# Performance work log

Measured on AMD Instinct MI355X. Metric: run time of the kernel, lower is better.

The kernel has to match this reference:

```python
import jax, jax.numpy as jnp
import numpy as np

HEADS = 6
DIM_HEAD = 64
SCALE = DIM_HEAD ** -0.5
BN_EPS = 1e-5


def _dw_pw(x, w_dw, gamma, beta, mean, var, w_pw, stride):
    """Depthwise 3x3 conv (groups=C) -> BatchNorm (inference) -> 1x1 pointwise conv."""
    C = x.shape[1]
    y = jax.lax.conv_general_dilated(
        x, w_dw, window_strides=(stride, stride), padding=((1, 1), (1, 1)),
        dimension_numbers=('NCHW', 'OIHW', 'NCHW'), feature_group_count=C)
    inv = gamma / jnp.sqrt(var + BN_EPS)
    y = y * inv[None, :, None, None] + (beta - mean * inv)[None, :, None, None]
    # 1x1 conv as einsum: w_pw is [O, C]
    return jnp.einsum('bchw,oc->bohw', y, w_pw)


def setup_inputs() -> dict:
    key = jax.random.key(0)
    ks = jax.random.split(key, 10)
    B, C, H, W = 32, 384, 32, 32
    inner = HEADS * DIM_HEAD  # 384
    ws = 0.05  # weight scale to keep attention logits sane
    return {
        'x': jax.random.normal(ks[0], (B, C, H, W), jnp.float32),
        'q_dw': jax.random.normal(ks[1], (C, 1, 3, 3), jnp.float32) * ws,
        'q_gamma': jnp.ones((C,), jnp.float32),
        'q_beta': jnp.zeros((C,), jnp.float32),
        'q_mean': jax.random.normal(ks[2], (C,), jnp.float32) * 0.1,
        'q_var': jax.random.uniform(ks[3], (C,), jnp.float32) + 0.5,
        'q_pw': jax.random.normal(ks[4], (inner, C), jnp.float32) * ws,
        'kv_dw': jax.random.normal(ks[5], (C, 1, 3, 3), jnp.float32) * ws,
        'kv_gamma': jnp.ones((C,), jnp.float32),
        'kv_beta': jnp.zeros((C,), jnp.float32),
        'kv_mean': jax.random.normal(ks[6], (C,), jnp.float32) * 0.1,
        'kv_var': jax.random.uniform(ks[7], (C,), jnp.float32) + 0.5,
        'kv_pw': jax.random.normal(ks[8], (2 * inner, C), jnp.float32) * ws,
        'out_w': jax.random.normal(ks[9], (C, inner), jnp.float32) * ws,
        'out_b': jnp.zeros((C,), jnp.float32),
    }


def reference(x, q_dw, q_gamma, q_beta, q_mean, q_var, q_pw,
              kv_dw, kv_gamma, kv_beta, kv_mean, kv_var, kv_pw,
              out_w, out_b):
    B, C, H, W = x.shape
    h, d = HEADS, DIM_HEAD
    # Q at full resolution, K/V spatially downsampled (stride 2)
    q = _dw_pw(x, q_dw, q_gamma, q_beta, q_mean, q_var, q_pw, stride=1)   # [B, h*d, H, W]
    kv = _dw_pw(x, kv_dw, kv_gamma, kv_beta, kv_mean, kv_var, kv_pw, stride=2)  # [B, 2*h*d, Hk, Wk]
    k, v = jnp.split(kv, 2, axis=1)
    Hk, Wk = k.shape[2], k.shape[3]
    # 'b (h d) x y -> b h (x y) d'
    q = q.reshape(B, h, d, H * W).transpose(0, 1, 3, 2)
    k = k.reshape(B, h, d, Hk * Wk).transpose(0, 1, 3, 2)
    v = v.reshape(B, h, d, Hk * Wk).transpose(0, 1, 3, 2)
    dots = jnp.einsum('bhid,bhjd->bhij', q, k) * SCALE  # [B, h, HW, HkWk]
    attn = jax.nn.softmax(dots, axis=-1)
    out = jnp.einsum('bhij,bhjd->bhid', attn, v)        # [B, h, HW, d]
    # 'b h (x y) d -> b (h d) x y'
    out = out.transpose(0, 1, 3, 2).reshape(B, h * d, H, W)
    # final 1x1 conv projection (dropout is identity, p=0)
    return jnp.einsum('bchw,oc->bohw', out, out_w) + out_b[None, :, None, None]
```

## Files before the change

kernel.cpp:

```cpp
#include <hip/hip_runtime.h>
#include <hip/hip_bf16.h>

#define CIN 384
#define PQ 1024
#define PKV 256
#define HEADS 6
#define DH 64
#define INNER 384
#define ATTN_SCALE 0.125f

typedef __hip_bfloat16 bf16;
typedef unsigned short ushort;
typedef __bf16 bf16x8 __attribute__((ext_vector_type(8)));
typedef float floatx4 __attribute__((ext_vector_type(4)));

__device__ __forceinline__ float b2f(bf16 v) { return __bfloat162float(v); }
__device__ __forceinline__ bf16 f2b(float v) { return __float2bfloat16(v); }
__device__ __forceinline__ ushort f2bu(float v) { bf16 h = __float2bfloat16(v); return *(ushort*)&h; }
__device__ __forceinline__ float ldf(const void* p, size_t i, int isbf) {
    return isbf ? __bfloat162float(((const bf16*)p)[i]) : ((const float*)p)[i];
}
__device__ __forceinline__ void dma16(const bf16* g, bf16* l) {
    __builtin_amdgcn_global_load_lds(
        (const __attribute__((address_space(1))) unsigned int*)g,
        (__attribute__((address_space(3))) unsigned int*)l, 16, 0, 0);
}
__device__ __forceinline__ int probe_isbf(const void* x) {
    const unsigned* u = (const unsigned*)x;
    int cnt = 0;
    for (int i = 0; i < 64; i++) {
        unsigned e = (u[i] >> 7) & 0xFFu;
        cnt += (e >= 100u && e <= 140u) ? 1 : 0;
    }
    return cnt >= 48 ? 1 : 0;
}
__device__ __forceinline__ unsigned cvtpk(float lo, float hi) {
    unsigned r;
    asm("v_cvt_pk_bf16_f32 %0, %1, %2" : "=v"(r) : "v"(lo), "v"(hi));
    return r;
}
__device__ __forceinline__ void halfswap(unsigned a, unsigned b, unsigned& lo, unsigned& hi) {
#if __has_builtin(__builtin_amdgcn_permlane32_swap)
    auto r = __builtin_amdgcn_permlane32_swap(a, b, false, false);
    lo = r[0]; hi = r[1];
#else
    unsigned ax = (unsigned)__shfl_xor((int)a, 32, 64);
    unsigned bx = (unsigned)__shfl_xor((int)b, 32, 64);
    bool lower = (threadIdx.x & 32) == 0;
    lo = lower ? a : bx;
    hi = lower ? ax : b;
#endif
}

template <int STRIDE, int G, int HO, int WO>
__device__ __forceinline__ void dw_bn_body(
        const void* __restrict__ x, const void* __restrict__ wdw,
        const void* __restrict__ gamma, const void* __restrict__ beta,
        const void* __restrict__ mean, const void* __restrict__ var,
        bf16* __restrict__ yt, int isbf, int rg, int c0, int b, int tid,
        char* smem) {
    constexpr int IN_ROWS = (G - 1) * STRIDE + 3;
    constexpr int PT = G * WO;
    float* xs = (float*)smem;
    ushort (*outt)[40] = (ushort (*)[40])smem;

    int ri0 = rg * G * STRIDE - 1;

    const int NCHUNK = 32 * IN_ROWS * 4;
    for (int ch = tid; ch < NCHUNK; ch += 256) {
        int wc = ch & 3;
        int cc = (ch >> 2) & 31;
        int i  = ch >> 7;
        int row = ri0 + i;
        float f[8];
        if (row >= 0 && row < 32) {
            size_t goff = ((size_t)(b * CIN + c0 + cc) * 32 + row) * 32 + wc * 8;
            if (isbf) {
                uint4 v = *(const uint4*)((const bf16*)x + goff);
                const ushort* u = (const ushort*)&v;
#pragma unroll
                for (int j = 0; j < 8; j++) f[j] = __uint_as_float((unsigned)u[j] << 16);
            } else {
                float4 v0 = *(const float4*)((const float*)x + goff);
                float4 v1 = *(const float4*)((const float*)x + goff + 4);
                f[0] = v0.x; f[1] = v0.y; f[2] = v0.z; f[3] = v0.w;
                f[4] = v1.x; f[5] = v1.y; f[6] = v1.z; f[7] = v1.w;
            }
        } else {
#pragma unroll
            for (int j = 0; j < 8; j++) f[j] = 0.f;
        }
        float* rb = xs + ((size_t)(i * 32 + cc)) * 32;
        int key = cc & 7;
        float4 fa = {f[0], f[1], f[2], f[3]};
        float4 fb = {f[4], f[5], f[6], f[7]};
        *(float4*)(rb + ((2 * wc) ^ key) * 4)     = fa;
        *(float4*)(rb + ((2 * wc + 1) ^ key) * 4) = fb;
    }

    int cc = tid & 31;
    int g  = tid >> 5;
    int c  = c0 + cc;
    int key = cc & 7;
    float w9[9];
#pragma unroll
    for (int k = 0; k < 9; k++) w9[k] = ldf(wdw, c * 9 + k, isbf);
    float inv  = ldf(gamma, c, isbf) * rsqrtf(ldf(var, c, isbf) + 1e-5f);
    float bias = ldf(beta, c, isbf) - ldf(mean, c, isbf) * inv;
    __syncthreads();

    float o[STRIDE == 1 ? 32 : 8];
    if (STRIDE == 1) {
#pragma unroll
        for (int p = 0; p < 2; p++) {
            float rf[3][18];
#pragma unroll
            for (int ky = 0; ky < 3; ky++) {
                const float* rb = xs + ((size_t)((g + ky) * 32 + cc)) * 32;
#pragma unroll
                for (int cch = 0; cch < 4; cch++) {
                    float4 v = *(const float4*)(rb + ((4 * p + cch) ^ key) * 4);
                    rf[ky][1 + 4 * cch] = v.x; rf[ky][2 + 4 * cch] = v.y;
                    rf[ky][3 + 4 * cch] = v.z; rf[ky][4 + 4 * cch] = v.w;
                }
                rf[ky][0]  = p ? rb[((3 ^ key) * 4) + 3] : 0.f;
                rf[ky][17] = p ? 0.f : rb[((4 ^ key) * 4) + 0];
            }
#pragma unroll
            for (int j = 0; j < 16; j++) {
                float acc = w9[0] * rf[0][j] + w9[1] * rf[0][j + 1] + w9[2] * rf[0][j + 2]
                          + w9[3] * rf[1][j] + w9[4] * rf[1][j + 1] + w9[5] * rf[1][j + 2]
                          + w9[6] * rf[2][j] + w9[7] * rf[2][j + 1] + w9[8] * rf[2][j + 2];
                o[p * 16 + j] = acc * inv + bias;
            }
        }
    } else {
        int rgrp = g & 3, hf = g >> 2;
        float rf[3][17];
#pragma unroll
        for (int ky = 0; ky < 3; ky++) {
            const float* rb = xs + ((size_t)((2 * rgrp + ky) * 32 + cc)) * 32;
#pragma unroll
            for (int cch = 0; cch < 4; cch++) {
                float4 v = *(const float4*)(rb + ((4 * hf + cch) ^ key) * 4);
                rf[ky][1 + 4 * cch] = v.x; rf[ky][2 + 4 * cch] = v.y;
                rf[ky][3 + 4 * cch] = v.z; rf[ky][4 + 4 * cch] = v.w;
            }
            rf[ky][0] = hf ? rb[((3 ^ key) * 4) + 3] : 0.f;
        }
#pragma unroll
        for (int j = 0; j < 8; j++) {
            float acc = w9[0] * rf[0][2 * j] + w9[1] * rf[0][2 * j + 1] + w9[2] * rf[0][2 * j + 2]
                      + w9[3] * rf[1][2 * j] + w9[4] * rf[1][2 * j + 1] + w9[5] * rf[1][2 * j + 2]
                      + w9[6] * rf[2][2 * j] + w9[7] * rf[2][2 * j + 1] + w9[8] * rf[2][2 * j + 2];
            o[j] = acc * inv + bias;
        }
    }
    __syncthreads();

    if (STRIDE == 1) {
#pragma unroll
        for (int wo = 0; wo < 32; wo++) outt[g * WO + wo][cc] = f2bu(o[wo]);
    } else {
        int rgrp = g & 3, hf = g >> 2;
#pragma unroll
        for (int j = 0; j < 8; j++) outt[rgrp * 16 + hf * 8 + j][cc] = f2bu(o[j]);
    }
    __syncthreads();

    const size_t pbase = (size_t)b * (HO * WO) + (size_t)rg * G * WO;
    for (int chk = tid; chk < PT * 4; chk += 256) {
        int k = chk & 3, p = chk >> 2;
        uint4 v = *(const uint4*)&outt[p][k * 8];
        *(uint4*)(yt + (pbase + p) * CIN + c0 + k * 8) = v;
    }
}

__global__ __launch_bounds__(256) void dw_bn_all(
        const void* __restrict__ x,
        const void* __restrict__ q_dw, const void* __restrict__ q_gamma,
        const void* __restrict__ q_beta, const void* __restrict__ q_mean,
        const void* __restrict__ q_var, bf16* __restrict__ yqt,
        const void* __restrict__ kv_dw, const void* __restrict__ kv_gamma,
        const void* __restrict__ kv_beta, const void* __restrict__ kv_mean,
        const void* __restrict__ kv_var, bf16* __restrict__ ykvt,
        const void* __restrict__ w0, const void* __restrict__ w1,
        const void* __restrict__ w2, bf16* __restrict__ wdst) {
    __shared__ __align__(16) char smem[40960];
    int isbf = probe_isbf(x);
    int rg = blockIdx.x;
    int y  = blockIdx.y;
    int b  = blockIdx.z;
    int tid = threadIdx.x;

    if (y < 12) {
        dw_bn_body<1, 8, 32, 32>(x, q_dw, q_gamma, q_beta, q_mean, q_var,
                                 yqt, isbf, rg, y * 32, b, tid, smem);
    } else if (y == 12) {
        const int n0 = INNER * CIN, n1 = 2 * INNER * CIN, n2 = INNER * CIN;
        const int total = n0 + n1 + n2;
        for (int i = (b * 4 + rg) * 256 + tid; i < total; i += 32768) {
            float v;
            if (i < n0) v = ldf(w0, i, isbf);
            else if (i < n0 + n1) v = ldf(w1, i - n0, isbf);
            else v = ldf(w2, i - n0 - n1, isbf);
            wdst[i] = f2b(v);
        }
    } else {
        dw_bn_body<2, 4, 16, 16>(x, kv_dw, kv_gamma, kv_beta, kv_mean, kv_var,
                                 ykvt, isbf, rg, (y - 13) * 32, b, tid, smem);
    }
}

__global__ __launch_bounds__(256, 3) void mfma_pw_qkv(
        const bf16* __restrict__ qpw, const bf16* __restrict__ yqt,
        bf16* __restrict__ qalt,
        const bf16* __restrict__ kvpw, const bf16* __restrict__ ykvt,
        bf16* __restrict__ kalt, bf16* __restrict__ valt) {
    __shared__ __align__(16) bf16 As[2][4096];
    __shared__ __align__(16) bf16 Bs[2][4096];
    int tid = threadIdx.x;
    int wave = tid >> 6, lane = tid & 63;
    int l15 = lane & 15, quad = lane >> 4;
    int wm = wave & 1, wn = wave >> 1;

    int bid = blockIdx.x;
    int P, b, p0, o0;
    const bf16 *asrc0, *bsrc0;
    bf16* outq;
    if (bid < 768) {
        int m = bid;
        int p0t = m & 7; m >>= 3;
        int o0t = m % 3; b = m / 3;
        P = 1024; p0 = p0t * 128; o0 = o0t * 128;
        asrc0 = yqt; bsrc0 = qpw; outq = qalt;
    } else {
        int m = bid - 768;
        int p0t = m & 1; m >>= 1;
        int o0t = m % 6; b = m / 6;
        P = 256; p0 = p0t * 128; o0 = o0t * 128;
        asrc0 = ykvt; bsrc0 = kvpw; outq = kalt;
    }

    const bf16* asrc = asrc0 + ((size_t)b * P + p0) * CIN;
    const bf16* bsrc = bsrc0 + (size_t)o0 * CIN;

    int srow = (lane >> 2);
    int sc   = lane & 3;
    auto stage = [&](int step, int buf) {
#pragma unroll
        for (int it = 0; it < 2; it++) {
            int row = wave * 32 + it * 16 + srow;
            int g = sc ^ (row & 3);
            size_t goff = (size_t)row * CIN + step * 32 + g * 8;
            dma16(asrc + goff, &As[buf][(wave * 2 + it) * 512]);
            dma16(bsrc + goff, &Bs[buf][(wave * 2 + it) * 512]);
        }
    };

    floatx4 acc[4][4];
#pragma unroll
    for (int pt = 0; pt < 4; pt++)
#pragma unroll
        for (int ot = 0; ot < 4; ot++) acc[pt][ot] = (floatx4){0.f, 0.f, 0.f, 0.f};

    stage(0, 0);
    __syncthreads();
    for (int s = 0; s < CIN / 32; s++) {
        int buf = s & 1;
        if (s < CIN / 32 - 1) stage(s + 1, buf ^ 1);
        bf16x8 af[4], bw[4];
        int slot = (quad ^ (l15 & 3)) * 8;
#pragma unroll
        for (int pt = 0; pt < 4; pt++)
            af[pt] = *(const bf16x8*)&As[buf][(wm * 64 + pt * 16 + l15) * 32 + slot];
#pragma unroll
        for (int ot = 0; ot < 4; ot++)
            bw[ot] = *(const bf16x8*)&Bs[buf][(wn * 64 + ot * 16 + l15) * 32 + slot];
#pragma unroll
        for (int pt = 0; pt < 4; pt++)
#pragma unroll
            for (int ot = 0; ot < 4; ot++)
                acc[pt][ot] = __builtin_amdgcn_mfma_f32_16x16x32_bf16(af[pt], bw[ot], acc[pt][ot], 0, 0, 0);
        __syncthreads();
    }

    int pw0 = p0 + wm * 64, ow0 = o0 + wn * 64;
#pragma unroll
    for (int ot = 0; ot < 4; ot++) {
        int o = ow0 + ot * 16 + l15;
        if (o < INNER) {
            int h = o >> 6, d = o & 63;
            bf16* base = outq + ((size_t)(b * HEADS + h) * P) * 64 + d;
#pragma unroll
            for (int pt = 0; pt < 4; pt++)
#pragma unroll
                for (int r = 0; r < 4; r++)
                    base[(size_t)(pw0 + pt * 16 + quad * 4 + r) * 64] = f2b(acc[pt][ot][r]);
        } else {
            int ch = o - INNER;
            bf16* base = valt + ((size_t)b * INNER + ch) * PKV;
#pragma unroll
            for (int pt = 0; pt < 4; pt++)
#pragma unroll
                for (int r = 0; r < 4; r++)
                    base[pw0 + pt * 16 + quad * 4 + r] = f2b(acc[pt][ot][r]);
        }
    }
}

__global__ __launch_bounds__(256, 3) void mfma_pw_out(
        const bf16* __restrict__ wt, const bf16* __restrict__ yt,
        const void* __restrict__ bias, void* __restrict__ out0,
        const void* __restrict__ xprobe) {
    __shared__ __align__(16) bf16 As[2][4096];
    __shared__ __align__(16) bf16 Bs[2][4096];
    const int P = PQ, O = CIN;
    int tid = threadIdx.x;
    int wave = tid >> 6, lane = tid & 63;
    int l15 = lane & 15, quad = lane >> 4;
    int wm = wave & 1, wn = wave >> 1;
    int b = blockIdx.z;
    int p0 = blockIdx.x * 128;
    int o0 = blockIdx.y * 128;

    const bf16* asrc = yt + ((size_t)b * P + p0) * CIN;
    const bf16* bsrc = wt + (size_t)o0 * CIN;

    int srow = (lane >> 2);
    int sc   = lane & 3;
    auto stage = [&](int step, int buf) {
#pragma unroll
        for (int it = 0; it < 2; it++) {
            int row = wave * 32 + it * 16 + srow;
            int g = sc ^ (row & 3);
            size_t goff = (size_t)row * CIN + step * 32 + g * 8;
            dma16(asrc + goff, &As[buf][(wave * 2 + it) * 512]);
            dma16(bsrc + goff, &Bs[buf][(wave * 2 + it) * 512]);
        }
    };

    floatx4 acc[4][4];
#pragma unroll
    for (int pt = 0; pt < 4; pt++)
#pragma unroll
        for (int ot = 0; ot < 4; ot++) acc[pt][ot] = (floatx4){0.f, 0.f, 0.f, 0.f};

    stage(0, 0);
    __syncthreads();
    for (int s = 0; s < CIN / 32; s++) {
        int buf = s & 1;
        if (s < CIN / 32 - 1) stage(s + 1, buf ^ 1);
        bf16x8 af[4], bw[4];
        int slot = (quad ^ (l15 & 3)) * 8;
#pragma unroll
        for (int pt = 0; pt < 4; pt++)
            af[pt] = *(const bf16x8*)&As[buf][(wm * 64 + pt * 16 + l15) * 32 + slot];
#pragma unroll
        for (int ot = 0; ot < 4; ot++)
            bw[ot] = *(const bf16x8*)&Bs[buf][(wn * 64 + ot * 16 + l15) * 32 + slot];
#pragma unroll
        for (int pt = 0; pt < 4; pt++)
#pragma unroll
            for (int ot = 0; ot < 4; ot++)
                acc[pt][ot] = __builtin_amdgcn_mfma_f32_16x16x32_bf16(af[pt], bw[ot], acc[pt][ot], 0, 0, 0);
        __syncthreads();
    }

    int pw0 = p0 + wm * 64, ow0 = o0 + wn * 64;
    int isbf = probe_isbf(xprobe);
#pragma unroll
    for (int ot = 0; ot < 4; ot++) {
        int o = ow0 + ot * 16 + l15;
        float bv = ldf(bias, o, isbf);
#pragma unroll
        for (int pt = 0; pt < 4; pt++) {
            int p = pw0 + pt * 16 + quad * 4;
            size_t idx = ((size_t)b * O + o) * P + p;
            if (!isbf) {
                float4 v4 = {acc[pt][ot][0] + bv, acc[pt][ot][1] + bv,
                             acc[pt][ot][2] + bv, acc[pt][ot][3] + bv};
                *(float4*)((float*)out0 + idx) = v4;
            } else {
                ushort4 u4 = {f2bu(acc[pt][ot][0] + bv), f2bu(acc[pt][ot][1] + bv),
                              f2bu(acc[pt][ot][2] + bv), f2bu(acc[pt][ot][3] + bv)};
                *(ushort4*)((bf16*)out0 + idx) = u4;
            }
        }
    }
}

#define QKT(S, Q0, Q1)                                                              \
    do {                                                                            \
        floatx4 z_ = (floatx4){0.f, 0.f, 0.f, 0.f};                                 \
        _Pragma("unroll")                                                           \
        for (int jt_ = 0; jt_ < 16; jt_++) {                                        \
            int j_ = jt_ * 16 + l15;                                                \
            bf16x8 k0_ = *(const bf16x8*)&Kl[j_ * 64 + (quad ^ (j_ & 7)) * 8];      \
            bf16x8 k1_ = *(const bf16x8*)&Kl[j_ * 64 + ((4 + quad) ^ (j_ & 7)) * 8];\
            floatx4 t_ = __builtin_amdgcn_mfma_f32_16x16x32_bf16(k0_, Q0, z_, 0, 0, 0); \
            S[jt_] = __builtin_amdgcn_mfma_f32_16x16x32_bf16(k1_, Q1, t_, 0, 0, 0); \
        }                                                                           \
    } while (0)

#define SOFTMAX(S, PINV)                                                            \
    do {                                                                            \
        float m0_ = S[0][0], m1_ = S[0][1], m2_ = S[0][2], m3_ = S[0][3];           \
        _Pragma("unroll")                                                           \
        for (int jt_ = 1; jt_ < 16; jt_++) {                                        \
            m0_ = fmaxf(m0_, S[jt_][0]); m1_ = fmaxf(m1_, S[jt_][1]);               \
            m2_ = fmaxf(m2_, S[jt_][2]); m3_ = fmaxf(m3_, S[jt_][3]);               \
        }                                                                           \
        float mx_ = fmaxf(fmaxf(m0_, m1_), fmaxf(m2_, m3_));                        \
        mx_ = fmaxf(mx_, __shfl_xor(mx_, 16, 64));                                  \
        mx_ = fmaxf(mx_, __shfl_xor(mx_, 32, 64));                                  \
        float mc_ = mx_ * C;                                                        \
        float a0_ = 0.f, a1_ = 0.f, a2_ = 0.f, a3_ = 0.f;                           \
        _Pragma("unroll")                                                           \
        for (int jt_ = 0; jt_ < 16; jt_++) {                                        \
            float e0_ = exp2f(S[jt_][0] * C - mc_);                                 \
            float e1_ = exp2f(S[jt_][1] * C - mc_);                                 \
            float e2_ = exp2f(S[jt_][2] * C - mc_);                                 \
            float e3_ = exp2f(S[jt_][3] * C - mc_);                                 \
            S[jt_][0] = e0_; S[jt_][1] = e1_; S[jt_][2] = e2_; S[jt_][3] = e3_;     \
            a0_ += e0_; a1_ += e1_; a2_ += e2_; a3_ += e3_;                         \
        }                                                                           \
        float sm_ = (a0_ + a1_) + (a2_ + a3_);                                      \
        sm_ += __shfl_xor(sm_, 16, 64);                                             \
        sm_ += __shfl_xor(sm_, 32, 64);                                             \
        PINV = 1.f / sm_;                                                           \
    } while (0)

#define PV_STORE(S, PINV, T)                                                        \
    do {                                                                            \
        floatx4 oacc_[4];                                                           \
        _Pragma("unroll")                                                           \
        for (int nt_ = 0; nt_ < 4; nt_++) oacc_[nt_] = (floatx4){0.f, 0.f, 0.f, 0.f}; \
        _Pragma("unroll")                                                           \
        for (int kk_ = 0; kk_ < 8; kk_++) {                                         \
            floatx4 se_ = S[2 * kk_], so_ = S[2 * kk_ + 1];                         \
            unsigned E0_ = cvtpk(se_[0] * PINV, se_[1] * PINV);                     \
            unsigned E1_ = cvtpk(se_[2] * PINV, se_[3] * PINV);                     \
            unsigned D0_ = cvtpk(so_[0] * PINV, so_[1] * PINV);                     \
            unsigned D1_ = cvtpk(so_[2] * PINV, so_[3] * PINV);                     \
            unsigned lo0_, hi0_, lo1_, hi1_;                                        \
            halfswap(E0_, D0_, lo0_, hi0_);                                         \
            halfswap(E1_, D1_, lo1_, hi1_);                                         \
            unsigned sel0_ = (quad & 1) ? hi0_ : lo0_;                              \
            unsigned sel1_ = (quad & 1) ? hi1_ : lo1_;                              \
            unsigned x0_ = (unsigned)__shfl_xor((int)sel0_, 16, 64);                \
            unsigned x1_ = (unsigned)__shfl_xor((int)sel1_, 16, 64);                \
            union { unsigned u[4]; bf16x8 v; } pf_;                                 \
            pf_.u[0] = (quad & 1) ? x0_ : sel0_;                                    \
            pf_.u[1] = (quad & 1) ? x1_ : sel1_;                                    \
            pf_.u[2] = (quad & 1) ? sel0_ : x0_;                                    \
            pf_.u[3] = (quad & 1) ? sel1_ : x1_;                                    \
            _Pragma("unroll")                                                       \
            for (int nt_ = 0; nt_ < 4; nt_++) {                                     \
                int d_ = nt_ * 16 + l15;                                            \
                bf16x8 bv_ = *(const bf16x8*)&Vl[d_ * 256 + ((kk_ * 4 + quad) ^ (d_ & 15)) * 8]; \
                oacc_[nt_] = __builtin_amdgcn_mfma_f32_16x16x32_bf16(pf_.v, bv_, oacc_[nt_], 0, 0, 0); \
            }                                                                       \
        }                                                                           \
        _Pragma("unroll")                                                           \
        for (int nt_ = 0; nt_ < 4; nt_++)                                           \
            _Pragma("unroll")                                                       \
            for (int r_ = 0; r_ < 4; r_++)                                          \
                Ot[wave][quad * 4 + r_][nt_ * 16 + l15] = f2bu(oacc_[nt_][r_]);     \
        int row_ = lane >> 2, d0_ = (lane & 3) * 16;                                \
        uint4 ld0_ = *(const uint4*)&Ot[wave][row_][d0_];                           \
        uint4 ld1_ = *(const uint4*)&Ot[wave][row_][d0_ + 8];                       \
        bf16* dst_ = ao + ((size_t)b * PQ + p0 + (T) * 64 + row_) * INNER + h * DH + d0_; \
        *(uint4*)dst_ = ld0_;                                                       \
        *(uint4*)(dst_ + 8) = ld1_;                                                 \
    } while (0)

__global__ __launch_bounds__(256, 2) void attn_kernel(
        const bf16* __restrict__ qalt, const bf16* __restrict__ kalt,
        const bf16* __restrict__ valt, bf16* __restrict__ ao) {
    __shared__ __align__(16) bf16 Kl[16384];
    __shared__ __align__(16) bf16 Vl[16384];
    __shared__ __align__(16) ushort Ot[4][16][80];
    int tid = threadIdx.x;
    int wave = tid >> 6, lane = tid & 63;
    int l15 = lane & 15, quad = lane >> 4;
    int blk = blockIdx.x;
    int swz = (blk & 7) * 96 + (blk >> 3);
    int seg = swz & 3;
    int bh  = swz >> 2;
    int b = bh / HEADS, h = bh % HEADS;

    const bf16* qbase = qalt + (size_t)(b * HEADS + h) * PQ * DH;
    const bf16* kbase = kalt + (size_t)(b * HEADS + h) * PKV * DH;
    const bf16* vbase = valt + ((size_t)b * INNER + h * DH) * PKV;

    {
        int j = lane >> 3, cs = lane & 7;
#pragma unroll
        for (int it = 0; it < 8; it++) {
            int jr = (wave * 8 + it) * 8 + j;
            int g = cs ^ (jr & 7);
            dma16(kbase + (size_t)jr * 64 + g * 8, &Kl[(wave * 8 + it) * 512]);
        }
        int d = lane >> 5, cs2 = lane & 31;
#pragma unroll
        for (int it = 0; it < 8; it++) {
            int dr = (wave * 8 + it) * 2 + d;
            int g = cs2 ^ (dr & 15);
            dma16(vbase + (size_t)dr * 256 + g * 8, &Vl[(wave * 8 + it) * 512]);
        }
    }

    int p0 = seg * 256 + wave * 16;
    const bf16* qrow = qbase + (size_t)(p0 + l15) * DH + quad * 8;
    bf16x8 qA0 = *(const bf16x8*)qrow;
    bf16x8 qA1 = *(const bf16x8*)(qrow + 32);
    bf16x8 qB0 = *(const bf16x8*)(qrow + 64 * DH);
    bf16x8 qB1 = *(const bf16x8*)(qrow + 64 * DH + 32);
    __syncthreads();

    const float C = ATTN_SCALE * 1.44269504f;
    floatx4 sA[16], sB[16];
    float pinv;

    QKT(sA, qA0, qA1);
    qA0 = *(const bf16x8*)(qrow + 128 * DH);
    qA1 = *(const bf16x8*)(qrow + 128 * DH + 32);

    SOFTMAX(sA, pinv);
    QKT(sB, qB0, qB1);
    PV_STORE(sA, pinv, 0);
    qB0 = *(const bf16x8*)(qrow + 192 * DH);
    qB1 = *(const bf16x8*)(qrow + 192 * DH + 32);

    SOFTMAX(sB, pinv);
    QKT(sA, qA0, qA1);
    PV_STORE(sB, pinv, 1);

    SOFTMAX(sA, pinv);
    QKT(sB, qB0, qB1);
    PV_STORE(sA, pinv, 2);

    SOFTMAX(sB, pinv);
    PV_STORE(sB, pinv, 3);
}

extern "C" void kernel_launch(void* const* d_in, const int* in_sizes, int n_in,
                              void* d_out, int out_size, void* d_ws, size_t ws_size,
                              hipStream_t stream) {
    const void* x        = d_in[0];
    const void* q_dw     = d_in[1];
    const void* q_gamma  = d_in[2];
    const void* q_beta   = d_in[3];
    const void* q_mean   = d_in[4];
    const void* q_var    = d_in[5];
    const void* q_pw     = d_in[6];
    const void* kv_dw    = d_in[7];
    const void* kv_gamma = d_in[8];
    const void* kv_beta  = d_in[9];
    const void* kv_mean  = d_in[10];
    const void* kv_var   = d_in[11];
    const void* kv_pw    = d_in[12];
    const void* out_w    = d_in[13];
    const void* out_b    = d_in[14];

    bf16* pool = (bf16*)((char*)d_ws + 256);
    bf16* yqt  = pool;
    bf16* ykvt = yqt  + (size_t)32 * 1024 * 384;
    bf16* qalt = ykvt + (size_t)32 * 256 * 384;
    bf16* kalt = qalt + (size_t)32 * 6 * 1024 * 64;
    bf16* valt = kalt + (size_t)32 * 6 * 256 * 64;
    bf16* wbf  = valt + (size_t)32 * 384 * 256;
    bf16* qpw_bf = wbf;
    bf16* kvpw_bf = wbf + (size_t)INNER * CIN;
    bf16* outw_bf = kvpw_bf + (size_t)2 * INNER * CIN;
    bf16* aob  = yqt;

    dw_bn_all<<<dim3(4, 25, 32), 256, 0, stream>>>(
        x, q_dw, q_gamma, q_beta, q_mean, q_var, yqt,
        kv_dw, kv_gamma, kv_beta, kv_mean, kv_var, ykvt,
        q_pw, kv_pw, out_w, wbf);
    mfma_pw_qkv<<<1152, 256, 0, stream>>>(qpw_bf, yqt, qalt, kvpw_bf, ykvt, kalt, valt);
    attn_kernel<<<768, 256, 0, stream>>>(qalt, kalt, valt, aob);
    mfma_pw_out<<<dim3(8, 3, 32), 256, 0, stream>>>(outw_bf, aob, out_b, d_out, x);
}
```

Before: 225.7 us.

## Stage depthwise conv input tile as bf16 in LDS to halve shared memory

The depthwise conv+BN kernel now stores its input halo tile in shared memory as packed bf16 instead of fp32, converting fp32 input with v_cvt_pk_bf16_f32 on load. The XOR swizzle is redone for 16-byte chunks of eight bf16 values, and the LDS allocation drops from 40 KB to 20 KB, which may let more blocks fit per CU and cuts LDS traffic. The format probe is also changed to read with 128-bit loads. In exchange, fp32 inputs are rounded to bf16 before the convolution, adding error on that path, and reads now need extra unpack operations.

```diff
diff --git a/kernel.cpp b/kernel.cpp
--- a/kernel.cpp
+++ b/kernel.cpp
@@ -26,11 +26,17 @@
         (__attribute__((address_space(3))) unsigned int*)l, 16, 0, 0);
 }
 __device__ __forceinline__ int probe_isbf(const void* x) {
-    const unsigned* u = (const unsigned*)x;
+    const uint4* p = (const uint4*)x;
     int cnt = 0;
-    for (int i = 0; i < 64; i++) {
-        unsigned e = (u[i] >> 7) & 0xFFu;
-        cnt += (e >= 100u && e <= 140u) ? 1 : 0;
+#pragma unroll
+    for (int i = 0; i < 16; i++) {
+        uint4 v = p[i];
+        const unsigned* u = (const unsigned*)&v;
+#pragma unroll
+        for (int j = 0; j < 4; j++) {
+            unsigned e = (u[j] >> 7) & 0xFFu;
+            cnt += (e >= 100u && e <= 140u) ? 1 : 0;
+        }
     }
     return cnt >= 48 ? 1 : 0;
 }
@@ -39,6 +45,8 @@
     asm("v_cvt_pk_bf16_f32 %0, %1, %2" : "=v"(r) : "v"(lo), "v"(hi));
     return r;
 }
+__device__ __forceinline__ float bflo(unsigned u) { return __uint_as_float(u << 16); }
+__device__ __forceinline__ float bfhi(unsigned u) { return __uint_as_float(u & 0xFFFF0000u); }
 __device__ __forceinline__ void halfswap(unsigned a, unsigned b, unsigned& lo, unsigned& hi) {
 #if __has_builtin(__builtin_amdgcn_permlane32_swap)
     auto r = __builtin_amdgcn_permlane32_swap(a, b, false, false);
@@ -61,7 +69,7 @@
         char* smem) {
     constexpr int IN_ROWS = (G - 1) * STRIDE + 3;
     constexpr int PT = G * WO;
-    float* xs = (float*)smem;
+    ushort* xs = (ushort*)smem;
     ushort (*outt)[40] = (ushort (*)[40])smem;
 
     int ri0 = rg * G * STRIDE - 1;
@@ -72,36 +80,25 @@
         int cc = (ch >> 2) & 31;
         int i  = ch >> 7;
         int row = ri0 + i;
-        float f[8];
+        uint4 v = {0u, 0u, 0u, 0u};
         if (row >= 0 && row < 32) {
             size_t goff = ((size_t)(b * CIN + c0 + cc) * 32 + row) * 32 + wc * 8;
             if (isbf) {
-                uint4 v = *(const uint4*)((const bf16*)x + goff);
-                const ushort* u = (const ushort*)&v;
-#pragma unroll
-                for (int j = 0; j < 8; j++) f[j] = __uint_as_float((unsigned)u[j] << 16);
+                v = *(const uint4*)((const bf16*)x + goff);
             } else {
                 float4 v0 = *(const float4*)((const float*)x + goff);
                 float4 v1 = *(const float4*)((const float*)x + goff + 4);
-                f[0] = v0.x; f[1] = v0.y; f[2] = v0.z; f[3] = v0.w;
-                f[4] = v1.x; f[5] = v1.y; f[6] = v1.z; f[7] = v1.w;
+                v.x = cvtpk(v0.x, v0.y); v.y = cvtpk(v0.z, v0.w);
+                v.z = cvtpk(v1.x, v1.y); v.w = cvtpk(v1.z, v1.w);
             }
-        } else {
-#pragma unroll
-            for (int j = 0; j < 8; j++) f[j] = 0.f;
-        }
-        float* rb = xs + ((size_t)(i * 32 + cc)) * 32;
-        int key = cc & 7;
-        float4 fa = {f[0], f[1], f[2], f[3]};
-        float4 fb = {f[4], f[5], f[6], f[7]};
-        *(float4*)(rb + ((2 * wc) ^ key) * 4)     = fa;
-        *(float4*)(rb + ((2 * wc + 1) ^ key) * 4) = fb;
+        }
+        *(uint4*)(xs + ((size_t)(i * 32 + cc)) * 32 + ((wc ^ (cc & 3)) * 8)) = v;
     }
 
     int cc = tid & 31;
     int g  = tid >> 5;
     int c  = c0 + cc;
-    int key = cc & 7;
+    int key = cc & 3;
     float w9[9];
 #pragma unroll
     for (int k = 0; k < 9; k++) w9[k] = ldf(wdw, c * 9 + k, isbf);
@@ -116,15 +113,20 @@
             float rf[3][18];
 #pragma unroll
             for (int ky = 0; ky < 3; ky++) {
-                const float* rb = xs + ((size_t)((g + ky) * 32 + cc)) * 32;
-#pragma unroll
-                for (int cch = 0; cch < 4; cch++) {
-                    float4 v = *(const float4*)(rb + ((4 * p + cch) ^ key) * 4);
-                    rf[ky][1 + 4 * cch] = v.x; rf[ky][2 + 4 * cch] = v.y;
-                    rf[ky][3 + 4 * cch] = v.z; rf[ky][4 + 4 * cch] = v.w;
+                const ushort* rb = xs + ((size_t)((g + ky) * 32 + cc)) * 32;
+                uint4 va = *(const uint4*)(rb + (((2 * p)     ^ key) * 8));
+                uint4 vb = *(const uint4*)(rb + (((2 * p + 1) ^ key) * 8));
+                const unsigned* ua = (const unsigned*)&va;
+                const unsigned* ub = (const unsigned*)&vb;
+#pragma unroll
+                for (int q = 0; q < 4; q++) {
+                    rf[ky][1 + 2 * q]  = bflo(ua[q]);
+                    rf[ky][2 + 2 * q]  = bfhi(ua[q]);
+                    rf[ky][9 + 2 * q]  = bflo(ub[q]);
+                    rf[ky][10 + 2 * q] = bfhi(ub[q]);
                 }
-                rf[ky][0]  = p ? rb[((3 ^ key) * 4) + 3] : 0.f;
-                rf[ky][17] = p ? 0.f : rb[((4 ^ key) * 4) + 0];
+                rf[ky][0]  = p ? bflo((unsigned)rb[((1 ^ key) * 8) + 7]) : 0.f;
+                rf[ky][17] = p ? 0.f : bflo((unsigned)rb[((2 ^ key) * 8) + 0]);
             }
 #pragma unroll
             for (int j = 0; j < 16; j++) {
@@ -139,14 +141,19 @@
         float rf[3][17];
 #pragma unroll
         for (int ky = 0; ky < 3; ky++) {
-            const float* rb = xs + ((size_t)((2 * rgrp + ky) * 32 + cc)) * 32;
-#pragma unroll
-            for (int cch = 0; cch < 4; cch++) {
-                float4 v = *(const float4*)(rb + ((4 * hf + cch) ^ key) * 4);
-                rf[ky][1 + 4 * cch] = v.x; rf[ky][2 + 4 * cch] = v.y;
-                rf[ky][3 + 4 * cch] = v.z; rf[ky][4 + 4 * cch] = v.w;
+            const ushort* rb = xs + ((size_t)((2 * rgrp + ky) * 32 + cc)) * 32;
+            uint4 va = *(const uint4*)(rb + (((2 * hf)     ^ key) * 8));
+            uint4 vb = *(const uint4*)(rb + (((2 * hf + 1) ^ key) * 8));
+            const unsigned* ua = (const unsigned*)&va;
+            const unsigned* ub = (const unsigned*)&vb;
+#pragma unroll
+            for (int q = 0; q < 4; q++) {
+                rf[ky][1 + 2 * q]  = bflo(ua[q]);
+                rf[ky][2 + 2 * q]  = bfhi(ua[q]);
+                rf[ky][9 + 2 * q]  = bflo(ub[q]);
+                rf[ky][10 + 2 * q] = bfhi(ub[q]);
             }
-            rf[ky][0] = hf ? rb[((3 ^ key) * 4) + 3] : 0.f;
+            rf[ky][0] = hf ? bflo((unsigned)rb[((1 ^ key) * 8) + 7]) : 0.f;
         }
 #pragma unroll
         for (int j = 0; j < 8; j++) {
@@ -186,7 +193,7 @@
         const void* __restrict__ kv_var, bf16* __restrict__ ykvt,
         const void* __restrict__ w0, const void* __restrict__ w1,
         const void* __restrict__ w2, bf16* __restrict__ wdst) {
-    __shared__ __align__(16) char smem[40960];
+    __shared__ __align__(16) char smem[20480];
     int isbf = probe_isbf(x);
     int rg = blockIdx.x;
     int y  = blockIdx.y;
```

Result: no change. 224.2 us (-0.7%).
